# Performance work log

Hardware: AMD Instinct MI355X
Metric: run time of the kernel (lower is better)

## Reference

```python
import jax, jax.numpy as jnp
import numpy as np

K_NEAREST = 16  # config.k_nearest_nodes (< num_nodes, so min() resolves to it)
EPS = 1e-6


def setup_inputs() -> dict:
    key = jax.random.key(0)
    k1, k2, k3 = jax.random.split(key, 3)
    N, M, F = 131072, 2048, 60
    center = jnp.array([0.0, 0.0, 1.3], dtype=jnp.float32)
    means = jax.random.normal(k1, (N, 3), dtype=jnp.float32) * 0.25 + center
    node_positions = jax.random.normal(k2, (M, 3), dtype=jnp.float32) * 0.3 + center
    node_offsets = jax.random.normal(k3, (F, M, 3), dtype=jnp.float32) * 0.01
    return {
        "means": means,
        "node_positions": node_positions,
        "node_offsets": node_offsets,
        "time_index": 5,
    }


def reference(means, node_positions, node_offsets, time_index):
    # torch.cdist (p=2): pairwise Euclidean distances [N, M]
    sq = (
        jnp.sum(means * means, axis=-1)[:, None]
        + jnp.sum(node_positions * node_positions, axis=-1)[None, :]
        - 2.0 * (means @ node_positions.T)
    )
    dist = jnp.maximum(jnp.sqrt(jnp.maximum(sq, 0.0)), EPS)  # .clamp_min(1e-6)

    # topk smallest -> top_k of negated distances
    neg_vals, inds = jax.lax.top_k(-dist, K_NEAREST)  # [N, K]
    vals = -neg_vals

    # softmax(-vals / (vals.mean().detach() + 1e-6))
    scale = jax.lax.stop_gradient(jnp.mean(vals)) + EPS
    weights = jax.nn.softmax(-vals / scale, axis=-1)  # [N, K]

    offsets = node_offsets[time_index][inds]  # gather: [N, K, 3]
    motion = jnp.einsum("nk,nkc->nc", weights, offsets)  # weighted reduce
    return means + motion
```

## Files before the change

### kernel.cpp

```cpp
#include <hip/hip_runtime.h>
#include <stdint.h>

#define M_NODES 2048
#define KSEL 16
#define BATCH 16
#define DBIAS 16.0f

typedef unsigned int u32;

#define CE_ASC(x, y)                    \
  {                                     \
    u32 _a = (x), _b = (y);             \
    (x) = min(_a, _b);                  \
    (y) = max(_a, _b);                  \
  }

template <int NQ>
__device__ __forceinline__ void oems_sort(u32* s) {
#pragma unroll
  for (int p = 1; p < NQ; p <<= 1) {
#pragma unroll
    for (int k = p; k >= 1; k >>= 1) {
#pragma unroll
      for (int j = k & (p - 1); j + k < NQ; j += 2 * k) {
#pragma unroll
        for (int i = 0; i < k; ++i) {
          if ((i + j) / (2 * p) == (i + j + k) / (2 * p)) {
            CE_ASC(s[i + j], s[i + j + k])
          }
        }
      }
    }
  }
}

__device__ __forceinline__ void merge_into(u32 a[KSEL], const u32 s[KSEL]) {
#pragma unroll
  for (int i = 0; i < KSEL; ++i) {
    u32 sv = s[KSEL - 1 - i];
    a[i] = min(a[i], sv);
  }
#pragma unroll
  for (int st = 8; st >= 1; st >>= 1) {
#pragma unroll
    for (int i = 0; i < KSEL; ++i) {
      if ((i & st) == 0) {
        CE_ASC(a[i], a[i + st])
      }
    }
  }
}

__device__ __forceinline__ float key_to_dist(u32 k, float c ) {
  float kf = __uint_as_float(k & 0xFFFFF800u);
  float d2 = fmaxf(kf + c, 0.0f);
  return fmaxf(sqrtf(d2), 1e-6f);
}

__device__ __forceinline__ void select_scalar(float px, float py, float pz,
                                              const float* __restrict__ nodes,
                                              u32 a[KSEL], int jbase,
                                              int nbatch) {
  float pp = fmaf(px, px, fmaf(py, py, pz * pz));
  float cb = DBIAS - pp;
#pragma unroll
  for (int t = 0; t < KSEL; ++t) a[t] = 0xFFFFFFFFu;
#pragma unroll 1
  for (int b = 0; b < nbatch; ++b) {
    int j0 = jbase + BATCH * b;
    const float* np = nodes + 3 * j0;
    u32 s[BATCH];
#pragma unroll
    for (int u = 0; u < BATCH; ++u) {
      float nx = np[3 * u + 0], ny = np[3 * u + 1], nz = np[3 * u + 2];
      float dx = px - nx, dy = py - ny, dz = pz - nz;
      float d2 = fmaf(dx, dx, fmaf(dy, dy, dz * dz)) + cb;
      s[u] = (__float_as_uint(d2) & 0xFFFFF800u) | (u32)(j0 + u);
    }
    oems_sort<BATCH>(s);
    merge_into(a, s);
  }
}

__global__ __launch_bounds__(256) void k_pack(const float* __restrict__ nodes,
                                              float4* __restrict__ packed) {
  int i = blockIdx.x * blockDim.x + threadIdx.x;
  if (i < M_NODES) {
    float x = nodes[3 * i + 0], y = nodes[3 * i + 1], z = nodes[3 * i + 2];
    packed[i] = make_float4(x, y, z, fmaf(x, x, fmaf(y, y, z * z)) + DBIAS);
  }
}

template <bool STORE>
__global__ __launch_bounds__(256, 8) void k_select(
    const float* __restrict__ means, const float4* __restrict__ packed,
    u32* __restrict__ keys_out, float* __restrict__ sum_ptr, int N) {
  __shared__ u32 lists[3][64][KSEL + 1];

  int lane = threadIdx.x & 63;
  int w = __builtin_amdgcn_readfirstlane((int)(threadIdx.x >> 6));
  int n = blockIdx.x * 64 + lane;

  float px = means[3 * n + 0];
  float py = means[3 * n + 1];
  float pz = means[3 * n + 2];
  float m2x = -2.0f * px, m2y = -2.0f * py, m2z = -2.0f * pz;
  float pp = fmaf(px, px, fmaf(py, py, pz * pz));
  const u32 HMASK = 0xFFFFF800u;

  u32 t0[BATCH], t1[BATCH];
#pragma unroll
  for (int u = 0; u < BATCH; ++u) { t0[u] = 0xFFFFFFFFu; t1[u] = 0xFFFFFFFFu; }

  int jbase = 512 * w;
#pragma unroll 1
  for (int b = 0; b < 512 / BATCH; ++b) {
    int j0 = jbase + BATCH * b;
    const float4* np = packed + j0;
#pragma unroll
    for (int u = 0; u < BATCH; ++u) {
      float4 nd = np[u];
      float d2 = fmaf(nd.x, m2x, fmaf(nd.y, m2y, fmaf(nd.z, m2z, nd.w)));
      u32 key = (__float_as_uint(d2) & HMASK) | (u32)(j0 + u);
      t1[u] = min(max(t0[u], key), t1[u]);
      t0[u] = min(t0[u], key);
    }
  }

  u32 cand[2 * BATCH];
#pragma unroll
  for (int u = 0; u < BATCH; ++u) {
    cand[2 * u + 0] = t0[u];
    cand[2 * u + 1] = t1[u];
  }
  oems_sort<2 * BATCH>(cand);
  u32 a[KSEL];
#pragma unroll
  for (int t = 0; t < KSEL; ++t) a[t] = cand[t];

  if (w != 0) {
#pragma unroll
    for (int t = 0; t < KSEL; ++t) lists[w - 1][lane][t] = a[t];
  }
  __syncthreads();
  if (w != 0) return;

#pragma unroll 1
  for (int i = 0; i < 3; ++i) {
    u32 b2[KSEL];
#pragma unroll
    for (int t = 0; t < KSEL; ++t) b2[t] = lists[i][lane][t];
    merge_into(a, b2);
  }

  if (STORE) {
    u32* kp = keys_out + (size_t)n * KSEL;
#pragma unroll
    for (int t = 0; t < KSEL; t += 4) {
      *reinterpret_cast<uint4*>(kp + t) =
          make_uint4(a[t], a[t + 1], a[t + 2], a[t + 3]);
    }
  }

  float c = pp - DBIAS;
  float s = 0.0f;
#pragma unroll
  for (int t = 0; t < KSEL; ++t) s += key_to_dist(a[t], c);
#pragma unroll
  for (int off = 32; off > 0; off >>= 1) s += __shfl_xor(s, off);
  if (lane == 0) atomicAdd(sum_ptr, s);
}

template <bool RELOAD>
__global__ __launch_bounds__(256) void k_finish(
    const float* __restrict__ means, const float* __restrict__ nodes,
    const float* __restrict__ noffs, const int* __restrict__ tptr,
    const u32* __restrict__ keys, const float* __restrict__ sum_ptr,
    float* __restrict__ out, int N) {
  __shared__ float4 so[M_NODES];
  int ti = *tptr;
  {
    const float* src = noffs + (size_t)ti * (3 * M_NODES);
    for (int i = threadIdx.x; i < M_NODES; i += blockDim.x) {
      so[i] = make_float4(src[3 * i + 0], src[3 * i + 1], src[3 * i + 2], 0.0f);
    }
  }
  __syncthreads();

  int n = blockIdx.x * blockDim.x + threadIdx.x;
  float px = means[3 * n + 0];
  float py = means[3 * n + 1];
  float pz = means[3 * n + 2];
  float pp = fmaf(px, px, fmaf(py, py, pz * pz));
  float c = pp - DBIAS;

  u32 a[KSEL];
  if constexpr (!RELOAD) {
    select_scalar(px, py, pz, nodes, a, 0, M_NODES / BATCH);
  } else {
    const uint4* kp = reinterpret_cast<const uint4*>(keys + (size_t)n * KSEL);
#pragma unroll
    for (int t = 0; t < 4; ++t) {
      uint4 v = kp[t];
      a[4 * t + 0] = v.x; a[4 * t + 1] = v.y;
      a[4 * t + 2] = v.z; a[4 * t + 3] = v.w;
    }
  }

  float scale = (*sum_ptr) * (1.0f / ((float)N * (float)KSEL)) + 1e-6f;
  float inv = 1.0f / scale;
  float vmin = key_to_dist(a[0], c);

  float wsum = 0.0f, mx = 0.0f, my = 0.0f, mz = 0.0f;
#pragma unroll
  for (int t = 0; t < KSEL; ++t) {
    u32 k = a[t];
    float v = key_to_dist(k, c);
    float e = __expf((vmin - v) * inv);
    float4 o = so[k & 0x7FFu];
    wsum += e;
    mx = fmaf(e, o.x, mx);
    my = fmaf(e, o.y, my);
    mz = fmaf(e, o.z, mz);
  }
  float r = 1.0f / wsum;
  out[3 * n + 0] = px + mx * r;
  out[3 * n + 1] = py + my * r;
  out[3 * n + 2] = pz + mz * r;
}

__global__ __launch_bounds__(256, 8) void k_select_nows(
    const float* __restrict__ means, const float* __restrict__ nodes,
    float* __restrict__ sum_ptr, int N) {
  __shared__ u32 lists[3][64][KSEL + 1];
  int lane = threadIdx.x & 63;
  int w = __builtin_amdgcn_readfirstlane((int)(threadIdx.x >> 6));
  int n = blockIdx.x * 64 + lane;
  float px = means[3 * n + 0], py = means[3 * n + 1], pz = means[3 * n + 2];
  float pp = fmaf(px, px, fmaf(py, py, pz * pz));
  u32 a[KSEL];
  select_scalar(px, py, pz, nodes, a, 512 * w, 512 / BATCH);
  if (w != 0) {
#pragma unroll
    for (int t = 0; t < KSEL; ++t) lists[w - 1][lane][t] = a[t];
  }
  __syncthreads();
  if (w != 0) return;
#pragma unroll 1
  for (int i = 0; i < 3; ++i) {
    u32 b2[KSEL];
#pragma unroll
    for (int t = 0; t < KSEL; ++t) b2[t] = lists[i][lane][t];
    merge_into(a, b2);
  }
  float c = pp - DBIAS;
  float s = 0.0f;
#pragma unroll
  for (int t = 0; t < KSEL; ++t) s += key_to_dist(a[t], c);
#pragma unroll
  for (int off = 32; off > 0; off >>= 1) s += __shfl_xor(s, off);
  if (lane == 0) atomicAdd(sum_ptr, s);
}

extern "C" void kernel_launch(void* const* d_in, const int* in_sizes, int n_in,
                              void* d_out, int out_size, void* d_ws,
                              size_t ws_size, hipStream_t stream) {
  const float* means = (const float*)d_in[0];
  const float* nodes = (const float*)d_in[1];
  const float* noffs = (const float*)d_in[2];
  const int* tptr = (const int*)d_in[3];
  int N = in_sizes[0] / 3;

  float* sum_ptr = (float*)d_ws;
  float4* packed = (float4*)((char*)d_ws + 256);
  u32* keys = (u32*)((char*)d_ws + 256 + M_NODES * sizeof(float4));
  size_t need_pack = 256 + M_NODES * sizeof(float4);
  size_t need_full = need_pack + (size_t)N * KSEL * sizeof(u32);

  size_t zbytes = ws_size < 256 ? ws_size : 256;
  if (zbytes) hipMemsetAsync(d_ws, 0, zbytes, stream);

  dim3 blk(256);
  dim3 grid_sel((unsigned)((N + 63) / 64));
  dim3 grid_fin((unsigned)((N + 255) / 256));
  float* out = (float*)d_out;

  if (ws_size >= need_full) {
    k_pack<<<dim3(8), blk, 0, stream>>>(nodes, packed);
    k_select<true><<<grid_sel, blk, 0, stream>>>(means, packed, keys, sum_ptr, N);
    k_finish<true><<<grid_fin, blk, 0, stream>>>(means, nodes, noffs, tptr,
                                                 keys, sum_ptr, out, N);
  } else {
    k_select_nows<<<grid_sel, blk, 0, stream>>>(means, nodes, sum_ptr, N);
    k_finish<false><<<grid_fin, blk, 0, stream>>>(means, nodes, noffs, tptr,
                                                  keys, sum_ptr, out, N);
  }
}
```

Baseline: 87.53 us.

## Process two query points per lane in k_select to reuse node loads

Each lane of k_select now handles two query points (n and n+64), so every packed node float4 loaded is used for two distance evaluations and key updates. The grid is halved, shared lists double to hold both sets, and the launch bound drops from 8 to 4 waves to allow the doubled register state. This amortizes node-load and loop overhead but raises register pressure and halves the number of blocks, which may reduce occupancy and latency hiding.

```diff
diff --git a/kernel.cpp b/kernel.cpp
--- a/kernel.cpp
+++ b/kernel.cpp
@@ -92,25 +92,30 @@
 }
 
 template <bool STORE>
-__global__ __launch_bounds__(256, 8) void k_select(
+__global__ __launch_bounds__(256, 4) void k_select(
     const float* __restrict__ means, const float4* __restrict__ packed,
     u32* __restrict__ keys_out, float* __restrict__ sum_ptr, int N) {
-  __shared__ u32 lists[3][64][KSEL + 1];
+  __shared__ u32 lists[3][128][KSEL + 1];
 
   int lane = threadIdx.x & 63;
   int w = __builtin_amdgcn_readfirstlane((int)(threadIdx.x >> 6));
-  int n = blockIdx.x * 64 + lane;
-
-  float px = means[3 * n + 0];
-  float py = means[3 * n + 1];
-  float pz = means[3 * n + 2];
-  float m2x = -2.0f * px, m2y = -2.0f * py, m2z = -2.0f * pz;
-  float pp = fmaf(px, px, fmaf(py, py, pz * pz));
+  int n0 = blockIdx.x * 128 + lane;
+  int n1 = n0 + 64;
+
+  float p0x = means[3 * n0 + 0], p0y = means[3 * n0 + 1], p0z = means[3 * n0 + 2];
+  float p1x = means[3 * n1 + 0], p1y = means[3 * n1 + 1], p1z = means[3 * n1 + 2];
+  float a0x = -2.0f * p0x, a0y = -2.0f * p0y, a0z = -2.0f * p0z;
+  float a1x = -2.0f * p1x, a1y = -2.0f * p1y, a1z = -2.0f * p1z;
+  float pp0 = fmaf(p0x, p0x, fmaf(p0y, p0y, p0z * p0z));
+  float pp1 = fmaf(p1x, p1x, fmaf(p1y, p1y, p1z * p1z));
   const u32 HMASK = 0xFFFFF800u;
 
-  u32 t0[BATCH], t1[BATCH];
-#pragma unroll
-  for (int u = 0; u < BATCH; ++u) { t0[u] = 0xFFFFFFFFu; t1[u] = 0xFFFFFFFFu; }
+  u32 s0lo[BATCH], s0hi[BATCH], s1lo[BATCH], s1hi[BATCH];
+#pragma unroll
+  for (int u = 0; u < BATCH; ++u) {
+    s0lo[u] = 0xFFFFFFFFu; s0hi[u] = 0xFFFFFFFFu;
+    s1lo[u] = 0xFFFFFFFFu; s1hi[u] = 0xFFFFFFFFu;
+  }
 
   int jbase = 512 * w;
 #pragma unroll 1
@@ -120,52 +125,78 @@
 #pragma unroll
     for (int u = 0; u < BATCH; ++u) {
       float4 nd = np[u];
-      float d2 = fmaf(nd.x, m2x, fmaf(nd.y, m2y, fmaf(nd.z, m2z, nd.w)));
-      u32 key = (__float_as_uint(d2) & HMASK) | (u32)(j0 + u);
-      t1[u] = min(max(t0[u], key), t1[u]);
-      t0[u] = min(t0[u], key);
-    }
-  }
-
-  u32 cand[2 * BATCH];
-#pragma unroll
-  for (int u = 0; u < BATCH; ++u) {
-    cand[2 * u + 0] = t0[u];
-    cand[2 * u + 1] = t1[u];
-  }
-  oems_sort<2 * BATCH>(cand);
-  u32 a[KSEL];
-#pragma unroll
-  for (int t = 0; t < KSEL; ++t) a[t] = cand[t];
+      u32 tag = (u32)(j0 + u);
+      float d20 = fmaf(nd.x, a0x, fmaf(nd.y, a0y, fmaf(nd.z, a0z, nd.w)));
+      u32 k0 = (__float_as_uint(d20) & HMASK) | tag;
+      s0hi[u] = min(max(s0lo[u], k0), s0hi[u]);
+      s0lo[u] = min(s0lo[u], k0);
+      float d21 = fmaf(nd.x, a1x, fmaf(nd.y, a1y, fmaf(nd.z, a1z, nd.w)));
+      u32 k1 = (__float_as_uint(d21) & HMASK) | tag;
+      s1hi[u] = min(max(s1lo[u], k1), s1hi[u]);
+      s1lo[u] = min(s1lo[u], k1);
+    }
+  }
+
+  u32 a0[KSEL], a1[KSEL];
+  {
+    u32 cand[2 * BATCH];
+#pragma unroll
+    for (int u = 0; u < BATCH; ++u) {
+      cand[2 * u + 0] = s0lo[u];
+      cand[2 * u + 1] = s0hi[u];
+    }
+    oems_sort<2 * BATCH>(cand);
+#pragma unroll
+    for (int t = 0; t < KSEL; ++t) a0[t] = cand[t];
+#pragma unroll
+    for (int u = 0; u < BATCH; ++u) {
+      cand[2 * u + 0] = s1lo[u];
+      cand[2 * u + 1] = s1hi[u];
+    }
+    oems_sort<2 * BATCH>(cand);
+#pragma unroll
+    for (int t = 0; t < KSEL; ++t) a1[t] = cand[t];
+  }
 
   if (w != 0) {
 #pragma unroll
-    for (int t = 0; t < KSEL; ++t) lists[w - 1][lane][t] = a[t];
+    for (int t = 0; t < KSEL; ++t) {
+      lists[w - 1][lane][t] = a0[t];
+      lists[w - 1][lane + 64][t] = a1[t];
+    }
   }
   __syncthreads();
   if (w != 0) return;
 
 #pragma unroll 1
   for (int i = 0; i < 3; ++i) {
-    u32 b2[KSEL];
-#pragma unroll
-    for (int t = 0; t < KSEL; ++t) b2[t] = lists[i][lane][t];
-    merge_into(a, b2);
+    u32 b0[KSEL], b1[KSEL];
+#pragma unroll
+    for (int t = 0; t < KSEL; ++t) {
+      b0[t] = lists[i][lane][t];
+      b1[t] = lists[i][lane + 64][t];
+    }
+    merge_into(a0, b0);
+    merge_into(a1, b1);
   }
 
   if (STORE) {
-    u32* kp = keys_out + (size_t)n * KSEL;
+    u32* kp0 = keys_out + (size_t)n0 * KSEL;
+    u32* kp1 = keys_out + (size_t)n1 * KSEL;
 #pragma unroll
     for (int t = 0; t < KSEL; t += 4) {
-      *reinterpret_cast<uint4*>(kp + t) =
-          make_uint4(a[t], a[t + 1], a[t + 2], a[t + 3]);
-    }
-  }
-
-  float c = pp - DBIAS;
+      *reinterpret_cast<uint4*>(kp0 + t) =
+          make_uint4(a0[t], a0[t + 1], a0[t + 2], a0[t + 3]);
+      *reinterpret_cast<uint4*>(kp1 + t) =
+          make_uint4(a1[t], a1[t + 1], a1[t + 2], a1[t + 3]);
+    }
+  }
+
+  float c0 = pp0 - DBIAS, c1 = pp1 - DBIAS;
   float s = 0.0f;
 #pragma unroll
-  for (int t = 0; t < KSEL; ++t) s += key_to_dist(a[t], c);
+  for (int t = 0; t < KSEL; ++t)
+    s += key_to_dist(a0[t], c0) + key_to_dist(a1[t], c1);
 #pragma unroll
   for (int off = 32; off > 0; off >>= 1) s += __shfl_xor(s, off);
   if (lane == 0) atomicAdd(sum_ptr, s);
@@ -281,7 +312,7 @@
   if (zbytes) hipMemsetAsync(d_ws, 0, zbytes, stream);
 
   dim3 blk(256);
-  dim3 grid_sel((unsigned)((N + 63) / 64));
+  dim3 grid_sel((unsigned)((N + 127) / 128));
   dim3 grid_fin((unsigned)((N + 255) / 256));
   float* out = (float*)d_out;
 
@@ -291,7 +322,8 @@
     k_finish<true><<<grid_fin, blk, 0, stream>>>(means, nodes, noffs, tptr,
                                                  keys, sum_ptr, out, N);
   } else {
-    k_select_nows<<<grid_sel, blk, 0, stream>>>(means, nodes, sum_ptr, N);
+    dim3 grid_sel64((unsigned)((N + 63) / 64));
+    k_select_nows<<<grid_sel64, blk, 0, stream>>>(means, nodes, sum_ptr, N);
     k_finish<false><<<grid_fin, blk, 0, stream>>>(means, nodes, noffs, tptr,
                                                   keys, sum_ptr, out, N);
   }
```

Result: no change. 85.99 us (-1.8%).
